# Kernel optimization log

Hardware: AMD Instinct MI355X
Metric: run time of the kernel (lower is better)

## Reference

```python
import jax, jax.numpy as jnp
import numpy as np

D_MODEL = 1024
EXPAND = 2
D_INNER = D_MODEL * EXPAND
KERNEL = 4
EPS = 1e-5


def setup_inputs() -> dict:
    key = jax.random.key(0)
    ks = jax.random.split(key, 8)
    B, L = 2, 4096
    x = jax.random.normal(ks[0], (B, L, D_MODEL), dtype=jnp.float32)
    norm_w = jnp.ones((D_MODEL,), jnp.float32)
    norm_b = jnp.zeros((D_MODEL,), jnp.float32)
    # torch Linear weight layout [out, in]
    in_proj_w = jax.random.normal(ks[1], (2 * D_INNER, D_MODEL), jnp.float32) / np.sqrt(D_MODEL)
    # depthwise Conv1d weight [d_inner, 1, K]
    conv_w = jax.random.normal(ks[2], (D_INNER, 1, KERNEL), jnp.float32) / np.sqrt(KERNEL)
    conv_b = jax.random.normal(ks[3], (D_INNER,), jnp.float32) * 0.02
    gate_w = jax.random.normal(ks[4], (D_INNER, D_INNER), jnp.float32) / np.sqrt(D_INNER)
    gate_b = jnp.zeros((D_INNER,), jnp.float32)
    out_proj_w = jax.random.normal(ks[5], (D_MODEL, D_INNER), jnp.float32) / np.sqrt(D_INNER)
    return {"x": x, "norm_w": norm_w, "norm_b": norm_b, "in_proj_w": in_proj_w,
            "conv_w": conv_w, "conv_b": conv_b, "gate_w": gate_w, "gate_b": gate_b,
            "out_proj_w": out_proj_w}


def _layernorm(x, w, b):
    mu = jnp.mean(x, axis=-1, keepdims=True)
    var = jnp.var(x, axis=-1, keepdims=True)
    return (x - mu) * jax.lax.rsqrt(var + EPS) * w + b


def _glru(x, norm_w, norm_b, in_proj_w, conv_w, conv_b, gate_w, gate_b, out_proj_w):
    B, L, D = x.shape
    residual = x
    xn = _layernorm(x, norm_w, norm_b)
    xz = jnp.einsum('bld,ed->ble', xn, in_proj_w)  # [B,L,2*d_inner]
    x_inner, z = jnp.split(xz, 2, axis=-1)
    # causal depthwise conv: torch pads 3 both sides then slices [:L] == left-pad 3
    lhs = jnp.transpose(x_inner, (0, 2, 1))  # [B, C, L]
    conv = jax.lax.conv_general_dilated(
        lhs, conv_w, window_strides=(1,), padding=[(KERNEL - 1, 0)],
        feature_group_count=D_INNER,
        dimension_numbers=('NCH', 'OIH', 'NCH'))
    x_conv = jnp.transpose(conv, (0, 2, 1)) + conv_b  # [B, L, C]
    x_conv = jax.nn.silu(x_conv)
    a = jax.nn.sigmoid(jnp.einsum('blc,ec->ble', x_conv, gate_w) + gate_b)
    b = (1.0 - a) * x_conv
    # h_t = a_t * h_{t-1} + b_t, h_0 prior = 0 -> parallel associative scan
    def combine(e1, e2):
        a1, b1 = e1
        a2, b2 = e2
        return a1 * a2, a2 * b1 + b2
    _, y = jax.lax.associative_scan(combine, (a, b), axis=1)
    y = y * jax.nn.silu(z)
    return residual + jnp.einsum('blc,dc->bld', y, out_proj_w)


def reference(x, norm_w, norm_b, in_proj_w, conv_w, conv_b, gate_w, gate_b, out_proj_w):
    return _glru(x, norm_w, norm_b, in_proj_w, conv_w, conv_b, gate_w, gate_b, out_proj_w)
```

## Files before the change

kernel.cpp:

```cpp
#include <hip/hip_runtime.h>
#include <cstdint>

#define D_MODEL 1024
#define D_INNER 2048
#define LSEQ    4096
#define BATCH   2
#define M_ROWS  (BATCH * LSEQ)
#define CHUNK   128
#define NCHUNK  (LSEQ / CHUNK)

typedef unsigned short u16;
typedef __bf16 bf16x8 __attribute__((ext_vector_type(8)));
typedef float f32x4 __attribute__((ext_vector_type(4)));
typedef u16 u16x4 __attribute__((ext_vector_type(4)));

__device__ __forceinline__ u16 f2bf(float f) {
  union { float f; unsigned u; } x; x.f = f;
  unsigned u = x.u;
  unsigned r = (u + 0x7FFFu + ((u >> 16) & 1u)) >> 16;
  return (u16)r;
}
__device__ __forceinline__ float bf2f(u16 h) {
  union { unsigned u; float f; } x; x.u = ((unsigned)h) << 16;
  return x.f;
}
__device__ __forceinline__ float sigmoidf_(float v) { return 1.0f / (1.0f + expf(-v)); }
__device__ __forceinline__ float siluf_(float v)    { return v / (1.0f + expf(-v)); }

#define SBAR()   asm volatile("s_barrier" ::: "memory")
#define WAITL0() asm volatile("s_waitcnt lgkmcnt(0)" ::: "memory")

__global__ void __launch_bounds__(256)
cast3_kernel(const float* __restrict__ w0, const float* __restrict__ w1,
             const float* __restrict__ w2, u16* __restrict__ o0,
             u16* __restrict__ o1, u16* __restrict__ o2) {
  const int n04 = 2 * D_INNER * D_MODEL / 4;
  const int n14 = D_INNER * D_INNER / 4;
  const int n24 = D_MODEL * D_INNER / 4;
  int i = blockIdx.x * 256 + threadIdx.x;
  const float* src; u16* dst; int j;
  if (i < n04)            { src = w0; dst = o0; j = i; }
  else if (i < n04 + n14) { src = w1; dst = o1; j = i - n04; }
  else if (i < n04 + n14 + n24) { src = w2; dst = o2; j = i - n04 - n14; }
  else return;
  float4 v = ((const float4*)src)[j];
  u16x4 o;
  o.x = f2bf(v.x); o.y = f2bf(v.y); o.z = f2bf(v.z); o.w = f2bf(v.w);
  ((u16x4*)dst)[j] = o;
}

__global__ void __launch_bounds__(256)
ln_kernel(const float* __restrict__ x, const float* __restrict__ w,
          const float* __restrict__ b, u16* __restrict__ xn) {
  const int row = blockIdx.x;
  const int t = threadIdx.x;
  const float4 v = ((const float4*)(x + (size_t)row * D_MODEL))[t];
  float s  = v.x + v.y + v.z + v.w;
  float ss = v.x * v.x + v.y * v.y + v.z * v.z + v.w * v.w;
#pragma unroll
  for (int o = 32; o > 0; o >>= 1) {
    s  += __shfl_xor(s, o);
    ss += __shfl_xor(ss, o);
  }
  __shared__ float red[8];
  const int wid = t >> 6, lane = t & 63;
  if (lane == 0) { red[wid] = s; red[4 + wid] = ss; }
  __syncthreads();
  s  = red[0] + red[1] + red[2] + red[3];
  ss = red[4] + red[5] + red[6] + red[7];
  const float mu  = s * (1.0f / D_MODEL);
  const float var = ss * (1.0f / D_MODEL) - mu * mu;
  const float rs  = rsqrtf(var + 1e-5f);
  const float4 wv = ((const float4*)w)[t];
  const float4 bv = ((const float4*)b)[t];
  u16x4 o4;
  o4.x = f2bf((v.x - mu) * rs * wv.x + bv.x);
  o4.y = f2bf((v.y - mu) * rs * wv.y + bv.y);
  o4.z = f2bf((v.z - mu) * rs * wv.z + bv.z);
  o4.w = f2bf((v.w - mu) * rs * wv.w + bv.w);
  ((u16x4*)(xn + (size_t)row * D_MODEL))[t] = o4;
}

#define MFMA_BF16 __builtin_amdgcn_mfma_f32_16x16x32_bf16

template<int EPI, int BN>
__global__ void __launch_bounds__(512, 2)
gemmR(const u16* __restrict__ A, const u16* __restrict__ Bm,
      int M, int N, int K,
      const float* __restrict__ ef, float* __restrict__ of,
      u16* __restrict__ ob0, u16* __restrict__ ob1) {
  constexpr int NF  = BN / 64;
  constexpr int NBL = BN / 64;
  constexpr int BBY = BN * 128;
  __shared__ __align__(1024) char lds[65536 + 2 * BBY];
  const int tid = threadIdx.x, wid = tid >> 6, lane = tid & 63;
  const int nbx = N / BN;
  const int nwg = nbx * (M >> 8);
  const int bid = blockIdx.x;
  const int cpx = nwg >> 3;
  const int swzb = (bid & 7) * cpx + (bid >> 3);
  const int bx = swzb % nbx, by = swzb / nbx;
  const size_t m0 = (size_t)by << 8;
  const size_t n0 = (size_t)bx * BN;
  const int wr = wid >> 2, wc = wid & 3;
  const size_t rb = (size_t)K * 2;

  const int strow = lane >> 3;
  const int stchk = (lane & 7) ^ strow;
  const char* gA = (const char*)A  + (m0 + (size_t)(wid * 8 + strow)) * rb + stchk * 16;
  const char* gB = (const char*)Bm + (n0 + (size_t)(wid * 8 + strow)) * rb + stchk * 16;
  const int vb = wid * 1024 + lane * 16;

  const int q = lane >> 4, r15 = lane & 15;
  const int kx0 = ((q ^ (r15 & 7)) << 4);
  const int kx1 = (((4 + q) ^ (r15 & 7)) << 4);
  const int arow = (wr * 128 + r15) * 128;
  const int brow = (wc * (BN / 4) + r15) * 128;

  f32x4 acc[8][NF] = {};
  const int nk = K >> 6;
  bf16x8 rA[4], rB[NBL];

#pragma unroll
  for (int j = 0; j < 4; ++j)   rA[j] = *(const bf16x8*)(gA + (size_t)(j * 64) * rb);
#pragma unroll
  for (int j = 0; j < NBL; ++j) rB[j] = *(const bf16x8*)(gB + (size_t)(j * 64) * rb);
#pragma unroll
  for (int j = 0; j < 4; ++j)   *(bf16x8*)(lds + j * 8192 + vb) = rA[j];
#pragma unroll
  for (int j = 0; j < NBL; ++j) *(bf16x8*)(lds + 65536 + j * 8192 + vb) = rB[j];
  WAITL0();
  SBAR();

  size_t kb = 128;
  for (int t = 0; t < nk; ++t) {
    const int par = t & 1;
    const char* Ac = lds + par * 32768;
    const char* Bc = lds + 65536 + par * BBY;
    char* An = lds + (par ^ 1) * 32768;
    char* Bn = lds + 65536 + (par ^ 1) * BBY;
    const bool pf = (t + 1 < nk);

    if (pf) {
#pragma unroll
      for (int j = 0; j < 4; ++j)   rA[j] = *(const bf16x8*)(gA + kb + (size_t)(j * 64) * rb);
#pragma unroll
      for (int j = 0; j < NBL; ++j) rB[j] = *(const bf16x8*)(gB + kb + (size_t)(j * 64) * rb);
    }

    bf16x8 af[8], bfv[NF];
#pragma unroll
    for (int mf = 0; mf < 8; ++mf) af[mf] = *(const bf16x8*)(Ac + arow + mf * 2048 + kx0);
#pragma unroll
    for (int nf = 0; nf < NF; ++nf) bfv[nf] = *(const bf16x8*)(Bc + brow + nf * 2048 + kx0);
    __builtin_amdgcn_s_setprio(1);
#pragma unroll
    for (int mf = 0; mf < 8; ++mf)
#pragma unroll
      for (int nf = 0; nf < NF; ++nf)
        acc[mf][nf] = MFMA_BF16(af[mf], bfv[nf], acc[mf][nf], 0, 0, 0);
    __builtin_amdgcn_s_setprio(0);
#pragma unroll
    for (int mf = 0; mf < 8; ++mf) af[mf] = *(const bf16x8*)(Ac + arow + mf * 2048 + kx1);
#pragma unroll
    for (int nf = 0; nf < NF; ++nf) bfv[nf] = *(const bf16x8*)(Bc + brow + nf * 2048 + kx1);
    __builtin_amdgcn_s_setprio(1);
#pragma unroll
    for (int mf = 0; mf < 8; ++mf)
#pragma unroll
      for (int nf = 0; nf < NF; ++nf)
        acc[mf][nf] = MFMA_BF16(af[mf], bfv[nf], acc[mf][nf], 0, 0, 0);
    __builtin_amdgcn_s_setprio(0);

    if (pf) {
#pragma unroll
      for (int j = 0; j < 4; ++j)   *(bf16x8*)(An + j * 8192 + vb) = rA[j];
#pragma unroll
      for (int j = 0; j < NBL; ++j) *(bf16x8*)(Bn + j * 8192 + vb) = rB[j];
    }
    WAITL0();
    SBAR();
    kb += 128;
  }

  const int c0 = lane & 15;
  const int r0 = (lane >> 4) << 2;
  const bool isz = (EPI == 0) && (n0 >= (size_t)D_INNER);
#pragma unroll
  for (int mf = 0; mf < 8; ++mf) {
#pragma unroll
    for (int nf = 0; nf < NF; ++nf) {
#pragma unroll
      for (int rg = 0; rg < 4; ++rg) {
        const size_t row = m0 + (size_t)(wr * 128 + mf * 16 + r0 + rg);
        const size_t col = n0 + (size_t)(wc * (BN / 4) + nf * 16 + c0);
        const float v = acc[mf][nf][rg];
        if (EPI == 0) {
          if (!isz) ob0[row * D_INNER + col] = f2bf(v);
          else      ob1[row * D_INNER + (col - D_INNER)] = f2bf(siluf_(v));
        } else if (EPI == 1) {
          ob0[row * (size_t)N + col] = f2bf(v);
        } else {
          of[row * (size_t)N + col] = v + ef[row * (size_t)N + col];
        }
      }
    }
  }
}

__global__ void __launch_bounds__(256)
conv_silu_kernel(const u16* __restrict__ xin, const float* __restrict__ cw,
                 const float* __restrict__ cb, u16* __restrict__ xc) {
  const int c   = blockIdx.x * 256 + threadIdx.x;
  const int l0  = blockIdx.y * 8;
  const int bat = blockIdx.z;
  const size_t base = ((size_t)bat * LSEQ) * D_INNER + c;
  const float w0 = cw[c * 4 + 0], w1 = cw[c * 4 + 1], w2 = cw[c * 4 + 2], w3 = cw[c * 4 + 3];
  const float bb = cb[c];
  float v[11];
#pragma unroll
  for (int i = 0; i < 11; ++i) {
    const int l = l0 - 3 + i;
    v[i] = (l >= 0) ? bf2f(xin[base + (size_t)l * D_INNER]) : 0.0f;
  }
#pragma unroll
  for (int r = 0; r < 8; ++r) {
    const float acc = bb + w0 * v[r] + w1 * v[r + 1] + w2 * v[r + 2] + w3 * v[r + 3];
    xc[base + (size_t)(l0 + r) * D_INNER] = f2bf(siluf_(acc));
  }
}

__global__ void __launch_bounds__(256)
scan_a_kernel(const u16* __restrict__ g, const u16* __restrict__ xc,
              const float* __restrict__ gbias,
              float* __restrict__ cA, float* __restrict__ cB) {
  const int c   = (blockIdx.x * 256 + threadIdx.x) * 2;
  const int ch  = blockIdx.y;
  const int bat = blockIdx.z;
  const float bb0 = gbias[c], bb1 = gbias[c + 1];
  size_t idx = ((size_t)bat * LSEQ + (size_t)ch * CHUNK) * D_INNER + c;
  float pA0 = 1.0f, hB0 = 0.0f, pA1 = 1.0f, hB1 = 0.0f;
  for (int t = 0; t < CHUNK; ++t) {
    const ushort2 gg = *(const ushort2*)(g + idx);
    const ushort2 xx = *(const ushort2*)(xc + idx);
    const float a0 = sigmoidf_(bf2f(gg.x) + bb0);
    const float a1 = sigmoidf_(bf2f(gg.y) + bb1);
    pA0 *= a0; hB0 = a0 * hB0 + (1.0f - a0) * bf2f(xx.x);
    pA1 *= a1; hB1 = a1 * hB1 + (1.0f - a1) * bf2f(xx.y);
    idx += D_INNER;
  }
  const size_t o = ((size_t)bat * NCHUNK + ch) * D_INNER + c;
  *(float2*)(cA + o) = make_float2(pA0, pA1);
  *(float2*)(cB + o) = make_float2(hB0, hB1);
}

__global__ void __launch_bounds__(256)
scan_b_kernel(const float* __restrict__ cA, const float* __restrict__ cB,
              float* __restrict__ carry) {
  const int tid = blockIdx.x * 256 + threadIdx.x;
  const int bat = tid >> 11;
  const int c   = tid & (D_INNER - 1);
  float h = 0.0f;
  const size_t base = (size_t)bat * NCHUNK * D_INNER + c;
  for (int i = 0; i < NCHUNK; ++i) {
    const size_t o = base + (size_t)i * D_INNER;
    carry[o] = h;
    h = cA[o] * h + cB[o];
  }
}

__global__ void __launch_bounds__(256)
scan_c_kernel(const u16* __restrict__ g, const u16* __restrict__ xc,
              const u16* __restrict__ sz, const float* __restrict__ gbias,
              const float* __restrict__ carry, u16* __restrict__ yg) {
  const int c   = (blockIdx.x * 256 + threadIdx.x) * 2;
  const int ch  = blockIdx.y;
  const int bat = blockIdx.z;
  const float bb0 = gbias[c], bb1 = gbias[c + 1];
  const float2 h2 = *(const float2*)(carry + ((size_t)bat * NCHUNK + ch) * D_INNER + c);
  float h0 = h2.x, h1 = h2.y;
  size_t idx = ((size_t)bat * LSEQ + (size_t)ch * CHUNK) * D_INNER + c;
  for (int t = 0; t < CHUNK; ++t) {
    const ushort2 gg = *(const ushort2*)(g + idx);
    const ushort2 xx = *(const ushort2*)(xc + idx);
    const ushort2 zz = *(const ushort2*)(sz + idx);
    const float a0 = sigmoidf_(bf2f(gg.x) + bb0);
    const float a1 = sigmoidf_(bf2f(gg.y) + bb1);
    h0 = a0 * h0 + (1.0f - a0) * bf2f(xx.x);
    h1 = a1 * h1 + (1.0f - a1) * bf2f(xx.y);
    ushort2 o2;
    o2.x = f2bf(h0 * bf2f(zz.x));
    o2.y = f2bf(h1 * bf2f(zz.y));
    *(ushort2*)(yg + idx) = o2;
    idx += D_INNER;
  }
}

extern "C" void kernel_launch(void* const* d_in, const int* in_sizes, int n_in,
                              void* d_out, int out_size, void* d_ws, size_t ws_size,
                              hipStream_t stream) {
  const float* x         = (const float*)d_in[0];
  const float* norm_w    = (const float*)d_in[1];
  const float* norm_b    = (const float*)d_in[2];
  const float* in_proj_w = (const float*)d_in[3];
  const float* conv_w    = (const float*)d_in[4];
  const float* conv_b    = (const float*)d_in[5];
  const float* gate_w    = (const float*)d_in[6];
  const float* gate_b    = (const float*)d_in[7];
  const float* out_proj_w= (const float*)d_in[8];
  float* out = (float*)d_out;

  char* p = (char*)d_ws;
  u16* xn      = (u16*)p; p += (size_t)M_ROWS * D_MODEL * 2;
  u16* w_in    = (u16*)p; p += (size_t)2 * D_INNER * D_MODEL * 2;
  u16* w_gate  = (u16*)p; p += (size_t)D_INNER * D_INNER * 2;
  u16* w_out   = (u16*)p; p += (size_t)D_MODEL * D_INNER * 2;
  u16* x_inner = (u16*)p; p += (size_t)M_ROWS * D_INNER * 2;
  u16* szb     = (u16*)p; p += (size_t)M_ROWS * D_INNER * 2;
  u16* xconv   = (u16*)p; p += (size_t)M_ROWS * D_INNER * 2;
  u16* gbuf    = (u16*)p; p += (size_t)M_ROWS * D_INNER * 2;
  u16* yg      = (u16*)p; p += (size_t)M_ROWS * D_INNER * 2;
  float* cA    = (float*)p; p += (size_t)BATCH * NCHUNK * D_INNER * 4;
  float* cB    = (float*)p; p += (size_t)BATCH * NCHUNK * D_INNER * 4;
  float* carry = (float*)p; p += (size_t)BATCH * NCHUNK * D_INNER * 4;
  if ((size_t)(p - (char*)d_ws) > ws_size) return;

  const int ncast4 = (2 * D_INNER * D_MODEL + D_INNER * D_INNER + D_MODEL * D_INNER) / 4;
  cast3_kernel<<<dim3((ncast4 + 255) / 256), 256, 0, stream>>>(
      in_proj_w, gate_w, out_proj_w, w_in, w_gate, w_out);

  ln_kernel<<<dim3(M_ROWS), 256, 0, stream>>>(x, norm_w, norm_b, xn);

  gemmR<0, 256><<<dim3((M_ROWS / 256) * (2 * D_INNER / 256)), 512, 0, stream>>>(
      xn, w_in, M_ROWS, 2 * D_INNER, D_MODEL, nullptr, nullptr, x_inner, szb);

  conv_silu_kernel<<<dim3(D_INNER / 256, LSEQ / 8, BATCH), 256, 0, stream>>>(x_inner, conv_w, conv_b, xconv);

  gemmR<1, 256><<<dim3((M_ROWS / 256) * (D_INNER / 256)), 512, 0, stream>>>(
      xconv, w_gate, M_ROWS, D_INNER, D_INNER, nullptr, nullptr, gbuf, nullptr);

  scan_a_kernel<<<dim3(D_INNER / 512, NCHUNK, BATCH), 256, 0, stream>>>(gbuf, xconv, gate_b, cA, cB);
  scan_b_kernel<<<dim3(BATCH * D_INNER / 256), 256, 0, stream>>>(cA, cB, carry);
  scan_c_kernel<<<dim3(D_INNER / 512, NCHUNK, BATCH), 256, 0, stream>>>(gbuf, xconv, szb, gate_b, carry, yg);

  gemmR<2, 128><<<dim3((M_ROWS / 256) * (D_MODEL / 128)), 512, 0, stream>>>(
      yg, w_out, M_ROWS, D_MODEL, D_INNER, x, out, nullptr, nullptr);
}
```

Baseline: 341.2 us.

## Use direct global-to-LDS loads and interleave LDS reads with MFMA in GEMM

Replaces the register-staged global->LDS copy in the GEMM with global_load_lds direct loads, which removes the VGPR round trip and the ds_write instructions. It also splits each k-step into four MFMA quarter-blocks, with the LDS fragment reads and next-tile prefetch issues placed between them behind sched_barriers, so LDS reads overlap with matrix math. The LDS layout and the B-row mapping per wave change to fit the new load pattern. The risks are higher register pressure from the extra fragment buffers and correctness hazards with the vmcnt-only wait.

```diff
diff --git a/kernel.cpp b/kernel.cpp
--- a/kernel.cpp
+++ b/kernel.cpp
@@ -27,8 +27,15 @@
 __device__ __forceinline__ float sigmoidf_(float v) { return 1.0f / (1.0f + expf(-v)); }
 __device__ __forceinline__ float siluf_(float v)    { return v / (1.0f + expf(-v)); }
 
+__device__ __forceinline__ void gl_lds16(const void* g, void* l) {
+  __builtin_amdgcn_global_load_lds(
+      (const __attribute__((address_space(1))) void*)g,
+      (__attribute__((address_space(3))) void*)l, 16, 0, 0);
+}
+
 #define SBAR()   asm volatile("s_barrier" ::: "memory")
-#define WAITL0() asm volatile("s_waitcnt lgkmcnt(0)" ::: "memory")
+#define WAITV0() asm volatile("s_waitcnt vmcnt(0)" ::: "memory")
+#define SGB()    __builtin_amdgcn_sched_barrier(0)
 
 __global__ void __launch_bounds__(256)
 cast3_kernel(const float* __restrict__ w0, const float* __restrict__ w1,
@@ -85,13 +92,14 @@
 
 template<int EPI, int BN>
 __global__ void __launch_bounds__(512, 2)
-gemmR(const u16* __restrict__ A, const u16* __restrict__ Bm,
+gemmP(const u16* __restrict__ A, const u16* __restrict__ Bm,
       int M, int N, int K,
       const float* __restrict__ ef, float* __restrict__ of,
       u16* __restrict__ ob0, u16* __restrict__ ob1) {
   constexpr int NF  = BN / 64;
-  constexpr int NBL = BN / 64;
+  constexpr int NF2 = NF / 2;
   constexpr int BBY = BN * 128;
+  constexpr int BH  = BN / 128;
   __shared__ __align__(1024) char lds[65536 + 2 * BBY];
   const int tid = threadIdx.x, wid = tid >> 6, lane = tid & 63;
   const int nbx = N / BN;
@@ -109,79 +117,98 @@
   const int stchk = (lane & 7) ^ strow;
   const char* gA = (const char*)A  + (m0 + (size_t)(wid * 8 + strow)) * rb + stchk * 16;
   const char* gB = (const char*)Bm + (n0 + (size_t)(wid * 8 + strow)) * rb + stchk * 16;
-  const int vb = wid * 1024 + lane * 16;
+  const int sdw = wid * 1024;
+
+  auto ST_A = [&](int t) {
+    char* d = lds + (t & 1) * 32768 + sdw;
+    const char* s = gA + (size_t)t * 128;
+#pragma unroll
+    for (int h = 0; h < 2; ++h) {
+      gl_lds16(s + (size_t)(h * 128) * rb,      d + h * 16384);
+      gl_lds16(s + (size_t)(h * 128 + 64) * rb, d + h * 16384 + 8192);
+    }
+  };
+  auto ST_B = [&](int t) {
+    char* d = lds + 65536 + (t & 1) * BBY + sdw;
+    const char* s = gB + (size_t)t * 128;
+#pragma unroll
+    for (int h = 0; h < BH; ++h) {
+      gl_lds16(s + (size_t)(h * 128) * rb,      d + h * 16384);
+      gl_lds16(s + (size_t)(h * 128 + 64) * rb, d + h * 16384 + 8192);
+    }
+  };
 
   const int q = lane >> 4, r15 = lane & 15;
   const int kx0 = ((q ^ (r15 & 7)) << 4);
   const int kx1 = (((4 + q) ^ (r15 & 7)) << 4);
-  const int arow = (wr * 128 + r15) * 128;
-  const int brow = (wc * (BN / 4) + r15) * 128;
-
+  const int arow = r15 * 128;
+  const int bwoff = (BN == 256) ? ((wc >> 1) * 16384) : 0;
+  const int brow  = (BN == 256) ? (((wc & 1) * 64 + r15) * 128)
+                                : ((wc * 32 + r15) * 128);
+
+  bf16x8 af0[8], af1[8], b01[NF2], b23[NF2], c01[NF2], c23[NF2];
   f32x4 acc[8][NF] = {};
+
+#define RDA(dst, kx, base) _Pragma("unroll") \
+  for (int mf = 0; mf < 8; ++mf) dst[mf] = *(const bf16x8*)((base) + mf * 2048 + arow + (kx));
+#define RDB(dst, kx, base, nf0) _Pragma("unroll") \
+  for (int nf = 0; nf < NF2; ++nf) dst[nf] = *(const bf16x8*)((base) + (nf0 + nf) * 2048 + brow + (kx));
+#define MM(afr, bfr, nf0) do { __builtin_amdgcn_s_setprio(1); _Pragma("unroll") \
+  for (int mf = 0; mf < 8; ++mf) _Pragma("unroll") \
+    for (int nf = 0; nf < NF2; ++nf) \
+      acc[mf][nf0 + nf] = MFMA_BF16(afr[mf], bfr[nf], acc[mf][nf0 + nf], 0, 0, 0); \
+  __builtin_amdgcn_s_setprio(0); } while (0)
+
   const int nk = K >> 6;
-  bf16x8 rA[4], rB[NBL];
-
-#pragma unroll
-  for (int j = 0; j < 4; ++j)   rA[j] = *(const bf16x8*)(gA + (size_t)(j * 64) * rb);
-#pragma unroll
-  for (int j = 0; j < NBL; ++j) rB[j] = *(const bf16x8*)(gB + (size_t)(j * 64) * rb);
-#pragma unroll
-  for (int j = 0; j < 4; ++j)   *(bf16x8*)(lds + j * 8192 + vb) = rA[j];
-#pragma unroll
-  for (int j = 0; j < NBL; ++j) *(bf16x8*)(lds + 65536 + j * 8192 + vb) = rB[j];
-  WAITL0();
+
+  ST_A(0); ST_B(0);
+  WAITV0();
   SBAR();
-
-  size_t kb = 128;
+  {
+    const char* Ab = lds + wr * 16384;
+    const char* Bb = lds + 65536 + bwoff;
+    RDA(af0, kx0, Ab);
+    RDB(b01, kx0, Bb, 0);
+  }
+
   for (int t = 0; t < nk; ++t) {
-    const int par = t & 1;
-    const char* Ac = lds + par * 32768;
-    const char* Bc = lds + 65536 + par * BBY;
-    char* An = lds + (par ^ 1) * 32768;
-    char* Bn = lds + 65536 + (par ^ 1) * BBY;
+    const int p = t & 1;
+    const char* Ab = lds + p * 32768 + wr * 16384;
+    const char* Bb = lds + 65536 + p * BBY + bwoff;
+    const char* An = lds + (p ^ 1) * 32768 + wr * 16384;
+    const char* Bn = lds + 65536 + (p ^ 1) * BBY + bwoff;
     const bool pf = (t + 1 < nk);
 
+    if (pf) ST_A(t + 1);
+    RDB(b23, kx0, Bb, NF2);
+    SGB();
+    MM(af0, b01, 0);
+    SGB();
+
+    if (pf) ST_B(t + 1);
+    RDA(af1, kx1, Ab);
+    RDB(c01, kx1, Bb, 0);
+    SGB();
+    MM(af0, b23, NF2);
+    SGB();
+
+    RDB(c23, kx1, Bb, NF2);
+    SGB();
+    MM(af1, c01, 0);
+    SGB();
+
+    MM(af1, c23, NF2);
     if (pf) {
-#pragma unroll
-      for (int j = 0; j < 4; ++j)   rA[j] = *(const bf16x8*)(gA + kb + (size_t)(j * 64) * rb);
-#pragma unroll
-      for (int j = 0; j < NBL; ++j) rB[j] = *(const bf16x8*)(gB + kb + (size_t)(j * 64) * rb);
+      WAITV0();
+      SBAR();
+      RDA(af0, kx0, An);
+      RDB(b01, kx0, Bn, 0);
     }
-
-    bf16x8 af[8], bfv[NF];
-#pragma unroll
-    for (int mf = 0; mf < 8; ++mf) af[mf] = *(const bf16x8*)(Ac + arow + mf * 2048 + kx0);
-#pragma unroll
-    for (int nf = 0; nf < NF; ++nf) bfv[nf] = *(const bf16x8*)(Bc + brow + nf * 2048 + kx0);
-    __builtin_amdgcn_s_setprio(1);
-#pragma unroll
-    for (int mf = 0; mf < 8; ++mf)
-#pragma unroll
-      for (int nf = 0; nf < NF; ++nf)
-        acc[mf][nf] = MFMA_BF16(af[mf], bfv[nf], acc[mf][nf], 0, 0, 0);
-    __builtin_amdgcn_s_setprio(0);
-#pragma unroll
-    for (int mf = 0; mf < 8; ++mf) af[mf] = *(const bf16x8*)(Ac + arow + mf * 2048 + kx1);
-#pragma unroll
-    for (int nf = 0; nf < NF; ++nf) bfv[nf] = *(const bf16x8*)(Bc + brow + nf * 2048 + kx1);
-    __builtin_amdgcn_s_setprio(1);
-#pragma unroll
-    for (int mf = 0; mf < 8; ++mf)
-#pragma unroll
-      for (int nf = 0; nf < NF; ++nf)
-        acc[mf][nf] = MFMA_BF16(af[mf], bfv[nf], acc[mf][nf], 0, 0, 0);
-    __builtin_amdgcn_s_setprio(0);
-
-    if (pf) {
-#pragma unroll
-      for (int j = 0; j < 4; ++j)   *(bf16x8*)(An + j * 8192 + vb) = rA[j];
-#pragma unroll
-      for (int j = 0; j < NBL; ++j) *(bf16x8*)(Bn + j * 8192 + vb) = rB[j];
-    }
-    WAITL0();
-    SBAR();
-    kb += 128;
-  }
+  }
+
+#undef RDA
+#undef RDB
+#undef MM
 
   const int c0 = lane & 15;
   const int r0 = (lane >> 4) << 2;
@@ -331,18 +358,18 @@
 
   ln_kernel<<<dim3(M_ROWS), 256, 0, stream>>>(x, norm_w, norm_b, xn);
 
-  gemmR<0, 256><<<dim3((M_ROWS / 256) * (2 * D_INNER / 256)), 512, 0, stream>>>(
+  gemmP<0, 256><<<dim3((M_ROWS / 256) * (2 * D_INNER / 256)), 512, 0, stream>>>(
       xn, w_in, M_ROWS, 2 * D_INNER, D_MODEL, nullptr, nullptr, x_inner, szb);
 
   conv_silu_kernel<<<dim3(D_INNER / 256, LSEQ / 8, BATCH), 256, 0, stream>>>(x_inner, conv_w, conv_b, xconv);
 
-  gemmR<1, 256><<<dim3((M_ROWS / 256) * (D_INNER / 256)), 512, 0, stream>>>(
+  gemmP<1, 256><<<dim3((M_ROWS / 256) * (D_INNER / 256)), 512, 0, stream>>>(
       xconv, w_gate, M_ROWS, D_INNER, D_INNER, nullptr, nullptr, gbuf, nullptr);
 
   scan_a_kernel<<<dim3(D_INNER / 512, NCHUNK, BATCH), 256, 0, stream>>>(gbuf, xconv, gate_b, cA, cB);
   scan_b_kernel<<<dim3(BATCH * D_INNER / 256), 256, 0, stream>>>(cA, cB, carry);
   scan_c_kernel<<<dim3(D_INNER / 512, NCHUNK, BATCH), 256, 0, stream>>>(gbuf, xconv, szb, gate_b, carry, yg);
 
-  gemmR<2, 128><<<dim3((M_ROWS / 256) * (D_MODEL / 128)), 512, 0, stream>>>(
+  gemmP<2, 128><<<dim3((M_ROWS / 256) * (D_MODEL / 128)), 512, 0, stream>>>(
       yg, w_out, M_ROWS, D_MODEL, D_INNER, x, out, nullptr, nullptr);
 }
```

Measured after the change: 323.3 us. 1.06x faster.
